# Performance work log

Hardware: AMD Instinct MI355X
Metric: run time of the kernel (lower is better)

## Reference

```python
import jax, jax.numpy as jnp
import numpy as np

LATENT_DIM = 256
CODEBOOK_SIZE = 8192


def setup_inputs() -> dict:
    key = jax.random.key(0)
    k1, k2 = jax.random.split(key)
    z_e = jax.random.normal(k1, (16, 32, 32, LATENT_DIM), dtype=jnp.float32)
    codebook = jax.random.normal(k2, (CODEBOOK_SIZE, LATENT_DIM), dtype=jnp.float32)
    return {"z_e": z_e, "codebook": codebook}


def reference(z_e, codebook):
    orig_shape = z_e.shape
    z_flat = z_e.reshape(-1, LATENT_DIM)                      # [N, D]
    # squared distances via ||z||^2 + ||e||^2 - 2 z.e^T  -> [N, K]
    dists = (jnp.sum(z_flat ** 2, axis=1, keepdims=True)
             + jnp.sum(codebook ** 2, axis=1)
             - 2.0 * jnp.matmul(z_flat, codebook.T))
    idx = jnp.argmin(dists, axis=1)                           # [N]
    z_q = codebook[idx].reshape(orig_shape)                   # gather + reshape
    commitment_loss = jnp.mean((jax.lax.stop_gradient(z_q) - z_e) ** 2)
    codebook_loss = jnp.mean((z_q - jax.lax.stop_gradient(z_e)) ** 2)
    loss = commitment_loss + codebook_loss
    z_q_st = z_e + jax.lax.stop_gradient(z_q - z_e)           # straight-through
    return (z_e, loss, z_q_st)
```

## Files before the change

kernel.cpp:

```cpp
#include <hip/hip_runtime.h>
#include <stdint.h>

typedef short short8 __attribute__((ext_vector_type(8)));
typedef float f32x4 __attribute__((ext_vector_type(4)));

#define DDIM 256
#define NROWS 16384
#define KCB 8192
#define KSPLIT 4
#define KC 2048
#define ND 4194304

__device__ __forceinline__ void gll16(const void* g, void* l) {
    __builtin_amdgcn_global_load_lds(
        (const __attribute__((address_space(1))) unsigned int*)g,
        (__attribute__((address_space(3))) unsigned int*)l, 16, 0, 0);
}

__device__ __forceinline__ unsigned short bf16_rne(float x) {
    unsigned u = __float_as_uint(x);
    unsigned r = (u + 0x7FFFu + ((u >> 16) & 1u)) >> 16;
    return (unsigned short)r;
}

__global__ void k_prep(const float* __restrict__ z, const float* __restrict__ cb,
                       unsigned short* __restrict__ zh, unsigned short* __restrict__ zl,
                       unsigned short* __restrict__ eh, unsigned short* __restrict__ el,
                       float* __restrict__ norms) {
    const int b = blockIdx.x, t = threadIdx.x;
    const bool isz = (b < 4096);
    const float* src = isz ? z : cb;
    unsigned short* hi = isz ? zh : eh;
    unsigned short* lo = isz ? zl : el;
    const int i = (isz ? b : (b - 4096)) * 256 + t;
    float4 v = reinterpret_cast<const float4*>(src)[i];
    ushort4 h, l;
    h.x = bf16_rne(v.x); l.x = bf16_rne(v.x - __uint_as_float((unsigned)h.x << 16));
    h.y = bf16_rne(v.y); l.y = bf16_rne(v.y - __uint_as_float((unsigned)h.y << 16));
    h.z = bf16_rne(v.z); l.z = bf16_rne(v.z - __uint_as_float((unsigned)h.z << 16));
    h.w = bf16_rne(v.w); l.w = bf16_rne(v.w - __uint_as_float((unsigned)h.w << 16));
    reinterpret_cast<ushort4*>(hi)[i] = h;
    reinterpret_cast<ushort4*>(lo)[i] = l;
    if (!isz) {
        float s = v.x * v.x + v.y * v.y + v.z * v.z + v.w * v.w;
#pragma unroll
        for (int off = 32; off > 0; off >>= 1) s += __shfl_xor(s, off, 64);
        if ((t & 63) == 0) norms[i >> 6] = s;
    }
}

__launch_bounds__(256, 2)
__global__ void k_score(const unsigned short* __restrict__ zh, const unsigned short* __restrict__ zl,
                        const unsigned short* __restrict__ eh, const unsigned short* __restrict__ el,
                        const float* __restrict__ norms,
                        float* __restrict__ cand_val, int* __restrict__ cand_idx) {
    __shared__ char smem[65536];

    const int rb = blockIdx.x;
    const int ks = blockIdx.y;
    const int t = threadIdx.x, w = t >> 6, lane = t & 63;
    const int l15 = lane & 15, l4 = lane >> 4;

    const int colq = t >> 3;
    const int voff0 = colq * 512 + (((t & 7) ^ (colq & 7)) * 16);

    int voffB[2];
#pragma unroll
    for (int kc = 0; kc < 2; ++kc)
        voffB[kc] = l15 * 128 + ((((kc * 4) + l4) ^ (lane & 7)) * 16);

    short8 Ah[2][8], Al[2][8];
    {
        const size_t base0 = ((size_t)(rb * 128 + w * 32 + l15)) * DDIM + l4 * 8;
#pragma unroll
        for (int r = 0; r < 2; ++r)
#pragma unroll
            for (int kk = 0; kk < 8; ++kk) {
                Ah[r][kk] = *reinterpret_cast<const short8*>(zh + base0 + r * 16 * DDIM + kk * 32);
                Al[r][kk] = *reinterpret_cast<const short8*>(zl + base0 + r * 16 * DDIM + kk * 32);
            }
    }

    const char* pe = (const char*)eh + (size_t)(ks * KC) * 512;
    const char* pl = (const char*)el + (size_t)(ks * KC) * 512;

    auto stage = [&](int s) {
        const int off = (s >> 2) * 32768 + (s & 3) * 128;
        char* sdst = smem + (s & 3) * 16384 + t * 16;
        gll16(pe + off + voff0,         sdst);
        gll16(pe + off + voff0 + 16384, sdst + 4096);
        gll16(pl + off + voff0,         sdst + 8192);
        gll16(pl + off + voff0 + 16384, sdst + 12288);
    };

    float v1[8], v2[8]; unsigned pk[8];
#pragma unroll
    for (int s = 0; s < 8; ++s) { v1[s] = 3.4e38f; v2[s] = 3.4e38f; pk[s] = 0; }

    f32x4 acc[2][4];

    auto compute = [&](int dc) {
        const char* cb0 = smem + dc * 16384;
        __builtin_amdgcn_s_setprio(1);
#pragma unroll
        for (int cf = 0; cf < 4; ++cf) {
#pragma unroll
            for (int kc = 0; kc < 2; ++kc) {
                short8 bh = *reinterpret_cast<const short8*>(cb0 + cf * 2048 + voffB[kc]);
                short8 bl = *reinterpret_cast<const short8*>(cb0 + 8192 + cf * 2048 + voffB[kc]);
                const int kk = dc * 2 + kc;
#pragma unroll
                for (int r = 0; r < 2; ++r) {
                    acc[r][cf] = __builtin_amdgcn_mfma_f32_16x16x32_bf16(Ah[r][kk], bh, acc[r][cf], 0, 0, 0);
                    acc[r][cf] = __builtin_amdgcn_mfma_f32_16x16x32_bf16(Ah[r][kk], bl, acc[r][cf], 0, 0, 0);
                    acc[r][cf] = __builtin_amdgcn_mfma_f32_16x16x32_bf16(Al[r][kk], bh, acc[r][cf], 0, 0, 0);
                }
            }
        }
        __builtin_amdgcn_s_setprio(0);
    };

    auto fold = [&](int ct) {
        const int nb = ks * KC + ct * 64 + l15;
        const float nn0 = norms[nb], nn1 = norms[nb + 16];
        const float nn2 = norms[nb + 32], nn3 = norms[nb + 48];
        const int cl0 = ct * 64 + l15;
#pragma unroll
        for (int r = 0; r < 2; ++r)
#pragma unroll
            for (int reg = 0; reg < 4; ++reg) {
                float s0 = fmaf(-2.f, acc[r][0][reg], nn0);
                float s1 = fmaf(-2.f, acc[r][1][reg], nn1);
                float s2 = fmaf(-2.f, acc[r][2][reg], nn2);
                float s3 = fmaf(-2.f, acc[r][3][reg], nn3);
                float sm = s0; int sj = cl0;
                if (s1 < sm) { sm = s1; sj = cl0 + 16; }
                if (s2 < sm) { sm = s2; sj = cl0 + 32; }
                if (s3 < sm) { sm = s3; sj = cl0 + 48; }
                const int s = r * 4 + reg;
                if (sm < v1[s]) { v2[s] = v1[s]; pk[s] = (pk[s] << 16) | (unsigned)sj; v1[s] = sm; }
                else if (sm < v2[s]) { v2[s] = sm; pk[s] = (pk[s] & 0xFFFFu) | ((unsigned)sj << 16); }
            }
    };

#define ACC_ZERO() do { \
    _Pragma("unroll") for (int r = 0; r < 2; ++r) \
    _Pragma("unroll") for (int cf = 0; cf < 4; ++cf) acc[r][cf] = (f32x4){0.f,0.f,0.f,0.f}; } while (0)

#define SYNC_V8()  do { asm volatile("s_waitcnt vmcnt(8) lgkmcnt(0)" ::: "memory"); \
    __builtin_amdgcn_sched_barrier(0); __builtin_amdgcn_s_barrier(); } while (0)
#define SYNC_V4()  do { asm volatile("s_waitcnt vmcnt(4) lgkmcnt(0)" ::: "memory"); \
    __builtin_amdgcn_sched_barrier(0); __builtin_amdgcn_s_barrier(); } while (0)
#define SYNC_V0()  do { asm volatile("s_waitcnt vmcnt(0) lgkmcnt(0)" ::: "memory"); \
    __builtin_amdgcn_sched_barrier(0); __builtin_amdgcn_s_barrier(); } while (0)

    stage(0); stage(1); stage(2);
    asm volatile("s_waitcnt vmcnt(8)" ::: "memory");
    __builtin_amdgcn_sched_barrier(0);
    __builtin_amdgcn_s_barrier();

#pragma unroll 1
    for (int ct = 0; ct < 31; ++ct) {
        ACC_ZERO();
        const int s0 = ct * 4;
#pragma unroll
        for (int dc = 0; dc < 4; ++dc) {
            stage(s0 + dc + 3);
            compute(dc);
            SYNC_V8();
        }
        fold(ct);
    }
    ACC_ZERO();
    stage(127); compute(0); SYNC_V8();
    compute(1);             SYNC_V4();
    compute(2);             SYNC_V0();
    compute(3);
    fold(31);

#pragma unroll
    for (int m = 1; m < 16; m <<= 1) {
#pragma unroll
        for (int s = 0; s < 8; ++s) {
            float ov1 = __shfl_xor(v1[s], m, 64);
            float ov2 = __shfl_xor(v2[s], m, 64);
            unsigned opk = (unsigned)__shfl_xor((int)pk[s], m, 64);
            const int ia = (int)(pk[s] & 0xFFFFu), ib = (int)(opk & 0xFFFFu);
            bool bl = (ov1 < v1[s]) || (ov1 == v1[s] && ib < ia);
            float f1 = bl ? ov1 : v1[s]; int fi = bl ? ib : ia;
            float rv = bl ? v1[s] : ov1; int ri = bl ? ia : ib;
            float sv = bl ? ov2 : v2[s]; int si = bl ? (int)(opk >> 16) : (int)(pk[s] >> 16);
            bool b2 = (sv < rv) || (sv == rv && si < ri);
            v1[s] = f1; v2[s] = b2 ? sv : rv;
            pk[s] = (unsigned)fi | ((unsigned)(b2 ? si : ri) << 16);
        }
    }
    __syncthreads();
    if (l15 == 0) {
#pragma unroll
        for (int s = 0; s < 8; ++s) {
            const int row = (s >> 2) * 16 + l4 * 4 + (s & 3);
            const int n = w * 32 + row;
            reinterpret_cast<int4*>(smem)[n] =
                make_int4(__float_as_int(v1[s]), (int)(pk[s] & 0xFFFFu),
                          __float_as_int(v2[s]), (int)(pk[s] >> 16));
        }
    }
    __syncthreads();
    if (t < 128) {
        int4 A = reinterpret_cast<int4*>(smem)[t];
        const int n = rb * 128 + t;
        cand_val[n * 8 + ks * 2 + 0] = __int_as_float(A.x);
        cand_val[n * 8 + ks * 2 + 1] = __int_as_float(A.z);
        cand_idx[n * 8 + ks * 2 + 0] = ks * KC + A.y;
        cand_idx[n * 8 + ks * 2 + 1] = ks * KC + A.w;
    }
}

__global__ void k_merge(const float* __restrict__ z, const float* __restrict__ cb,
                        const float* __restrict__ norms,
                        const float* __restrict__ cand_val, const int* __restrict__ cand_idx,
                        int* __restrict__ fidx) {
    const int gid = blockIdx.x * blockDim.x + threadIdx.x;
    const int wid = gid >> 6;
    const int lane = threadIdx.x & 63;
    float v1 = 3.4e38f, v2 = 3.4e38f; int i1 = 0, i2 = 0;
#pragma unroll
    for (int c = 0; c < 8; ++c) {
        float v = cand_val[wid * 8 + c]; int i = cand_idx[wid * 8 + c] & (KCB - 1);
        bool lt1 = (v < v1) || (v == v1 && i < i1);
        bool lt2 = (v < v2) || (v == v2 && i < i2);
        if (lt1) { v2 = v1; i2 = i1; v1 = v; i1 = i; }
        else if (lt2) { v2 = v; i2 = i; }
    }
    const float4 zq = *reinterpret_cast<const float4*>(z + (size_t)wid * DDIM + lane * 4);
    float d[2]; int ii[2] = { i1, i2 };
#pragma unroll
    for (int c = 0; c < 2; ++c) {
        const float4 e4 = *reinterpret_cast<const float4*>(cb + (size_t)ii[c] * DDIM + lane * 4);
        float s = zq.x * e4.x + zq.y * e4.y + zq.z * e4.z + zq.w * e4.w;
#pragma unroll
        for (int m = 32; m > 0; m >>= 1) s += __shfl_xor(s, m, 64);
        d[c] = norms[ii[c]] - 2.f * s;
    }
    const int best = (d[1] < d[0] || (d[1] == d[0] && ii[1] < ii[0])) ? ii[1] : ii[0];
    if (lane == 0) fidx[wid] = best;
}

__global__ void k_finalize(const float* __restrict__ z, const float* __restrict__ cb,
                           const int* __restrict__ fidx, float* __restrict__ out,
                           float* __restrict__ partials) {
    const int i4 = blockIdx.x * blockDim.x + threadIdx.x;
    float4 zv = *reinterpret_cast<const float4*>(z + (size_t)i4 * 4);
    *reinterpret_cast<float4*>(out + (size_t)i4 * 4) = zv;
    const int n = i4 >> 6;
    const int d0 = (i4 & 63) << 2;
    const int idx = fidx[n] & (KCB - 1);
    float4 q = *reinterpret_cast<const float4*>(cb + (size_t)idx * DDIM + d0);
    float* oq = out + (size_t)ND + 1 + (size_t)i4 * 4;
    oq[0] = q.x; oq[1] = q.y; oq[2] = q.z; oq[3] = q.w;
    const float dx = q.x - zv.x, dy = q.y - zv.y, dz = q.z - zv.z, dw = q.w - zv.w;
    float s = dx * dx + dy * dy + dz * dz + dw * dw;
#pragma unroll
    for (int off = 32; off > 0; off >>= 1) s += __shfl_xor(s, off, 64);
    __shared__ float sm[4];
    const int wv = threadIdx.x >> 6, ln = threadIdx.x & 63;
    if (ln == 0) sm[wv] = s;
    __syncthreads();
    if (threadIdx.x == 0) partials[blockIdx.x] = sm[0] + sm[1] + sm[2] + sm[3];
}

__global__ void k_loss(const float* __restrict__ partials, float* __restrict__ out) {
    float s = 0.f;
    for (int i = threadIdx.x; i < 4096; i += 256) s += partials[i];
#pragma unroll
    for (int off = 32; off > 0; off >>= 1) s += __shfl_xor(s, off, 64);
    __shared__ float sm[4];
    const int wv = threadIdx.x >> 6, ln = threadIdx.x & 63;
    if (ln == 0) sm[wv] = s;
    __syncthreads();
    if (threadIdx.x == 0) out[ND] = 2.0f * (sm[0] + sm[1] + sm[2] + sm[3]) / (float)ND;
}

extern "C" void kernel_launch(void* const* d_in, const int* in_sizes, int n_in,
                              void* d_out, int out_size, void* d_ws, size_t ws_size,
                              hipStream_t stream) {
    const float* z = (const float*)d_in[0];
    const float* cb = (const float*)d_in[1];
    float* out = (float*)d_out;
    float* ws = (float*)d_ws;

    float* norms = ws;
    int* fidx = (int*)(ws + 8192);
    float* partials = ws + 8192 + 16384;

    char* ob = (char*)d_out;
    unsigned short* zh = (unsigned short*)(ob);
    unsigned short* zl = (unsigned short*)(ob + 8388608);
    unsigned short* eh = (unsigned short*)(ob + 16777216);
    unsigned short* el = (unsigned short*)(ob + 20971520);
    float* cand_val = (float*)(ob + 25165824);
    int* cand_idx = (int*)(ob + 25690112);

    k_prep<<<dim3(6144), dim3(256), 0, stream>>>(z, cb, zh, zl, eh, el, norms);
    k_score<<<dim3(128, 4), dim3(256), 0, stream>>>(zh, zl, eh, el, norms, cand_val, cand_idx);
    k_merge<<<dim3(4096), dim3(256), 0, stream>>>(z, cb, norms, cand_val, cand_idx, fidx);
    k_finalize<<<dim3(4096), dim3(256), 0, stream>>>(z, cb, fidx, out, partials);
    k_loss<<<dim3(1), dim3(256), 0, stream>>>(partials, out);
}
```

Measured before the change: 266.0 us.

## Replace split-bf16 3-pass MFMA with single fp16 MFMA and top-3 exact rescoring

The scoring GEMM now quantizes z and the codebook once to fp16 and runs a single f16 MFMA per tile, replacing three bf16 hi/lo MFMAs. To make up for the lower precision, each split keeps top-3 candidates instead of top-2, and the merge kernel re-scores all 12 candidates exactly in fp32. Other changes: LDS staging is halved, codebook norms are staged into LDS, occupancy is raised to 3 blocks per CU, and candidate values are no longer written out. The risk is that fp16 error pushes the true argmin outside the top-3 per split, and the merge kernel now does six times more gathers.

```diff
diff --git a/kernel.cpp b/kernel.cpp
--- a/kernel.cpp
+++ b/kernel.cpp
@@ -1,7 +1,7 @@
 #include <hip/hip_runtime.h>
 #include <stdint.h>
 
-typedef short short8 __attribute__((ext_vector_type(8)));
+typedef _Float16 half8 __attribute__((ext_vector_type(8)));
 typedef float f32x4 __attribute__((ext_vector_type(4)));
 
 #define DDIM 256
@@ -17,30 +17,24 @@
         (__attribute__((address_space(3))) unsigned int*)l, 16, 0, 0);
 }
 
-__device__ __forceinline__ unsigned short bf16_rne(float x) {
-    unsigned u = __float_as_uint(x);
-    unsigned r = (u + 0x7FFFu + ((u >> 16) & 1u)) >> 16;
-    return (unsigned short)r;
+__device__ __forceinline__ unsigned short f2h(float x) {
+    union { _Float16 h; unsigned short u; } c;
+    c.h = (_Float16)x;
+    return c.u;
 }
 
 __global__ void k_prep(const float* __restrict__ z, const float* __restrict__ cb,
-                       unsigned short* __restrict__ zh, unsigned short* __restrict__ zl,
-                       unsigned short* __restrict__ eh, unsigned short* __restrict__ el,
+                       unsigned short* __restrict__ zf, unsigned short* __restrict__ ef,
                        float* __restrict__ norms) {
     const int b = blockIdx.x, t = threadIdx.x;
     const bool isz = (b < 4096);
     const float* src = isz ? z : cb;
-    unsigned short* hi = isz ? zh : eh;
-    unsigned short* lo = isz ? zl : el;
+    unsigned short* dst = isz ? zf : ef;
     const int i = (isz ? b : (b - 4096)) * 256 + t;
     float4 v = reinterpret_cast<const float4*>(src)[i];
-    ushort4 h, l;
-    h.x = bf16_rne(v.x); l.x = bf16_rne(v.x - __uint_as_float((unsigned)h.x << 16));
-    h.y = bf16_rne(v.y); l.y = bf16_rne(v.y - __uint_as_float((unsigned)h.y << 16));
-    h.z = bf16_rne(v.z); l.z = bf16_rne(v.z - __uint_as_float((unsigned)h.z << 16));
-    h.w = bf16_rne(v.w); l.w = bf16_rne(v.w - __uint_as_float((unsigned)h.w << 16));
-    reinterpret_cast<ushort4*>(hi)[i] = h;
-    reinterpret_cast<ushort4*>(lo)[i] = l;
+    ushort4 h;
+    h.x = f2h(v.x); h.y = f2h(v.y); h.z = f2h(v.z); h.w = f2h(v.w);
+    reinterpret_cast<ushort4*>(dst)[i] = h;
     if (!isz) {
         float s = v.x * v.x + v.y * v.y + v.z * v.z + v.w * v.w;
 #pragma unroll
@@ -49,12 +43,10 @@
     }
 }
 
-__launch_bounds__(256, 2)
-__global__ void k_score(const unsigned short* __restrict__ zh, const unsigned short* __restrict__ zl,
-                        const unsigned short* __restrict__ eh, const unsigned short* __restrict__ el,
-                        const float* __restrict__ norms,
-                        float* __restrict__ cand_val, int* __restrict__ cand_idx) {
-    __shared__ char smem[65536];
+__launch_bounds__(256, 3)
+__global__ void k_score(const unsigned short* __restrict__ zf, const unsigned short* __restrict__ ef,
+                        const float* __restrict__ norms, int* __restrict__ cand_idx) {
+    __shared__ char smem[40960];
 
     const int rb = blockIdx.x;
     const int ks = blockIdx.y;
@@ -69,77 +61,81 @@
     for (int kc = 0; kc < 2; ++kc)
         voffB[kc] = l15 * 128 + ((((kc * 4) + l4) ^ (lane & 7)) * 16);
 
-    short8 Ah[2][8], Al[2][8];
+    half8 A[2][8];
     {
         const size_t base0 = ((size_t)(rb * 128 + w * 32 + l15)) * DDIM + l4 * 8;
 #pragma unroll
         for (int r = 0; r < 2; ++r)
 #pragma unroll
-            for (int kk = 0; kk < 8; ++kk) {
-                Ah[r][kk] = *reinterpret_cast<const short8*>(zh + base0 + r * 16 * DDIM + kk * 32);
-                Al[r][kk] = *reinterpret_cast<const short8*>(zl + base0 + r * 16 * DDIM + kk * 32);
-            }
-    }
-
-    const char* pe = (const char*)eh + (size_t)(ks * KC) * 512;
-    const char* pl = (const char*)el + (size_t)(ks * KC) * 512;
+            for (int kk = 0; kk < 8; ++kk)
+                A[r][kk] = *reinterpret_cast<const half8*>(zf + base0 + r * 16 * DDIM + kk * 32);
+    }
+#pragma unroll
+    for (int r = 0; r < 2; ++r)
+#pragma unroll
+        for (int kk = 0; kk < 8; ++kk)
+            asm volatile("" : "+v"(A[r][kk]));
+
+    const char* pe = (const char*)ef + (size_t)(ks * KC) * 512;
+
+    gll16((const char*)(norms + ks * KC) + t * 16,        smem + 32768 + t * 16);
+    gll16((const char*)(norms + ks * KC) + 4096 + t * 16, smem + 32768 + 4096 + t * 16);
 
     auto stage = [&](int s) {
         const int off = (s >> 2) * 32768 + (s & 3) * 128;
-        char* sdst = smem + (s & 3) * 16384 + t * 16;
+        char* sdst = smem + (s & 3) * 8192 + t * 16;
         gll16(pe + off + voff0,         sdst);
         gll16(pe + off + voff0 + 16384, sdst + 4096);
-        gll16(pl + off + voff0,         sdst + 8192);
-        gll16(pl + off + voff0 + 16384, sdst + 12288);
     };
 
-    float v1[8], v2[8]; unsigned pk[8];
-#pragma unroll
-    for (int s = 0; s < 8; ++s) { v1[s] = 3.4e38f; v2[s] = 3.4e38f; pk[s] = 0; }
+    float v1[8], v2[8], v3[8]; unsigned pk[8]; int i3[8];
+#pragma unroll
+    for (int s = 0; s < 8; ++s) { v1[s] = 3.4e38f; v2[s] = 3.4e38f; v3[s] = 3.4e38f; pk[s] = 0; i3[s] = 0; }
 
     f32x4 acc[2][4];
 
     auto compute = [&](int dc) {
-        const char* cb0 = smem + dc * 16384;
+        const char* cb0 = smem + dc * 8192;
         __builtin_amdgcn_s_setprio(1);
 #pragma unroll
         for (int cf = 0; cf < 4; ++cf) {
 #pragma unroll
             for (int kc = 0; kc < 2; ++kc) {
-                short8 bh = *reinterpret_cast<const short8*>(cb0 + cf * 2048 + voffB[kc]);
-                short8 bl = *reinterpret_cast<const short8*>(cb0 + 8192 + cf * 2048 + voffB[kc]);
+                half8 b = *reinterpret_cast<const half8*>(cb0 + cf * 2048 + voffB[kc]);
                 const int kk = dc * 2 + kc;
 #pragma unroll
-                for (int r = 0; r < 2; ++r) {
-                    acc[r][cf] = __builtin_amdgcn_mfma_f32_16x16x32_bf16(Ah[r][kk], bh, acc[r][cf], 0, 0, 0);
-                    acc[r][cf] = __builtin_amdgcn_mfma_f32_16x16x32_bf16(Ah[r][kk], bl, acc[r][cf], 0, 0, 0);
-                    acc[r][cf] = __builtin_amdgcn_mfma_f32_16x16x32_bf16(Al[r][kk], bh, acc[r][cf], 0, 0, 0);
-                }
+                for (int r = 0; r < 2; ++r)
+                    acc[r][cf] = __builtin_amdgcn_mfma_f32_16x16x32_f16(A[r][kk], b, acc[r][cf], 0, 0, 0);
             }
         }
         __builtin_amdgcn_s_setprio(0);
     };
 
     auto fold = [&](int ct) {
-        const int nb = ks * KC + ct * 64 + l15;
-        const float nn0 = norms[nb], nn1 = norms[nb + 16];
-        const float nn2 = norms[nb + 32], nn3 = norms[nb + 48];
-        const int cl0 = ct * 64 + l15;
+        const float* nl = reinterpret_cast<const float*>(smem + 32768);
+        const int nb0 = ct * 64 + l15;
+        float nn[4];
+#pragma unroll
+        for (int c = 0; c < 4; ++c) nn[c] = nl[nb0 + c * 16];
 #pragma unroll
         for (int r = 0; r < 2; ++r)
 #pragma unroll
             for (int reg = 0; reg < 4; ++reg) {
-                float s0 = fmaf(-2.f, acc[r][0][reg], nn0);
-                float s1 = fmaf(-2.f, acc[r][1][reg], nn1);
-                float s2 = fmaf(-2.f, acc[r][2][reg], nn2);
-                float s3 = fmaf(-2.f, acc[r][3][reg], nn3);
-                float sm = s0; int sj = cl0;
-                if (s1 < sm) { sm = s1; sj = cl0 + 16; }
-                if (s2 < sm) { sm = s2; sj = cl0 + 32; }
-                if (s3 < sm) { sm = s3; sj = cl0 + 48; }
                 const int s = r * 4 + reg;
-                if (sm < v1[s]) { v2[s] = v1[s]; pk[s] = (pk[s] << 16) | (unsigned)sj; v1[s] = sm; }
-                else if (sm < v2[s]) { v2[s] = sm; pk[s] = (pk[s] & 0xFFFFu) | ((unsigned)sj << 16); }
+#pragma unroll
+                for (int c = 0; c < 4; ++c) {
+                    const float val = fmaf(-2.f, acc[r][c][reg], nn[c]);
+                    const int idx = nb0 + c * 16;
+                    const bool L1 = val < v1[s], L2 = val < v2[s], L3 = val < v3[s];
+                    const int oi1 = (int)(pk[s] & 0xFFFFu), oi2 = (int)(pk[s] >> 16);
+                    i3[s] = L2 ? oi2 : (L3 ? idx : i3[s]);
+                    v3[s] = L2 ? v2[s] : (L3 ? val : v3[s]);
+                    const int ni2 = L1 ? oi1 : (L2 ? idx : oi2);
+                    v2[s] = L1 ? v1[s] : (L2 ? val : v2[s]);
+                    const int ni1 = L1 ? idx : oi1;
+                    v1[s] = L1 ? val : v1[s];
+                    pk[s] = (unsigned)ni1 | ((unsigned)ni2 << 16);
+                }
             }
     };
 
@@ -147,15 +143,15 @@
     _Pragma("unroll") for (int r = 0; r < 2; ++r) \
     _Pragma("unroll") for (int cf = 0; cf < 4; ++cf) acc[r][cf] = (f32x4){0.f,0.f,0.f,0.f}; } while (0)
 
-#define SYNC_V8()  do { asm volatile("s_waitcnt vmcnt(8) lgkmcnt(0)" ::: "memory"); \
+#define SYNC_V4()  do { asm volatile("s_waitcnt vmcnt(4) lgkmcnt(0)" ::: "memory"); \
     __builtin_amdgcn_sched_barrier(0); __builtin_amdgcn_s_barrier(); } while (0)
-#define SYNC_V4()  do { asm volatile("s_waitcnt vmcnt(4) lgkmcnt(0)" ::: "memory"); \
+#define SYNC_V2()  do { asm volatile("s_waitcnt vmcnt(2) lgkmcnt(0)" ::: "memory"); \
     __builtin_amdgcn_sched_barrier(0); __builtin_amdgcn_s_barrier(); } while (0)
 #define SYNC_V0()  do { asm volatile("s_waitcnt vmcnt(0) lgkmcnt(0)" ::: "memory"); \
     __builtin_amdgcn_sched_barrier(0); __builtin_amdgcn_s_barrier(); } while (0)
 
     stage(0); stage(1); stage(2);
-    asm volatile("s_waitcnt vmcnt(8)" ::: "memory");
+    asm volatile("s_waitcnt vmcnt(4)" ::: "memory");
     __builtin_amdgcn_sched_barrier(0);
     __builtin_amdgcn_s_barrier();
 
@@ -167,13 +163,13 @@
         for (int dc = 0; dc < 4; ++dc) {
             stage(s0 + dc + 3);
             compute(dc);
-            SYNC_V8();
+            SYNC_V4();
         }
         fold(ct);
     }
     ACC_ZERO();
-    stage(127); compute(0); SYNC_V8();
-    compute(1);             SYNC_V4();
+    stage(127); compute(0); SYNC_V4();
+    compute(1);             SYNC_V2();
     compute(2);             SYNC_V0();
     compute(3);
     fold(31);
@@ -182,69 +178,68 @@
     for (int m = 1; m < 16; m <<= 1) {
 #pragma unroll
         for (int s = 0; s < 8; ++s) {
-            float ov1 = __shfl_xor(v1[s], m, 64);
-            float ov2 = __shfl_xor(v2[s], m, 64);
-            unsigned opk = (unsigned)__shfl_xor((int)pk[s], m, 64);
-            const int ia = (int)(pk[s] & 0xFFFFu), ib = (int)(opk & 0xFFFFu);
-            bool bl = (ov1 < v1[s]) || (ov1 == v1[s] && ib < ia);
-            float f1 = bl ? ov1 : v1[s]; int fi = bl ? ib : ia;
-            float rv = bl ? v1[s] : ov1; int ri = bl ? ia : ib;
-            float sv = bl ? ov2 : v2[s]; int si = bl ? (int)(opk >> 16) : (int)(pk[s] >> 16);
-            bool b2 = (sv < rv) || (sv == rv && si < ri);
-            v1[s] = f1; v2[s] = b2 ? sv : rv;
-            pk[s] = (unsigned)fi | ((unsigned)(b2 ? si : ri) << 16);
+            const float a1v = v1[s], a2v = v2[s], a3v = v3[s];
+            const int a1i = (int)(pk[s] & 0xFFFFu), a2i = (int)(pk[s] >> 16), a3i = i3[s];
+            const float b1v = __shfl_xor(a1v, m, 64), b2v = __shfl_xor(a2v, m, 64), b3v = __shfl_xor(a3v, m, 64);
+            const unsigned opk = (unsigned)__shfl_xor((int)pk[s], m, 64);
+            const int b1i = (int)(opk & 0xFFFFu), b2i = (int)(opk >> 16), b3i = __shfl_xor(a3i, m, 64);
+            auto lt = [](float va, int ia, float vb, int ib) { return va < vb || (va == vb && ia < ib); };
+            const bool w1 = lt(a1v, a1i, b1v, b1i);
+            const float c1v = w1 ? a1v : b1v; const int c1i = w1 ? a1i : b1i;
+            const float xav = w1 ? a2v : a1v; const int xai = w1 ? a2i : a1i;
+            const float xbv = w1 ? b1v : b2v; const int xbi = w1 ? b1i : b2i;
+            const bool w2 = lt(xav, xai, xbv, xbi);
+            const float c2v = w2 ? xav : xbv; const int c2i = w2 ? xai : xbi;
+            const float yav = w1 ? (w2 ? a3v : a2v) : (w2 ? a2v : a1v);
+            const int   yai = w1 ? (w2 ? a3i : a2i) : (w2 ? a2i : a1i);
+            const float ybv = w1 ? (w2 ? b1v : b2v) : (w2 ? b2v : b3v);
+            const int   ybi = w1 ? (w2 ? b1i : b2i) : (w2 ? b2i : b3i);
+            const bool w3 = lt(yav, yai, ybv, ybi);
+            v1[s] = c1v; v2[s] = c2v; v3[s] = w3 ? yav : ybv;
+            pk[s] = (unsigned)c1i | ((unsigned)c2i << 16);
+            i3[s] = w3 ? yai : ybi;
         }
     }
-    __syncthreads();
     if (l15 == 0) {
 #pragma unroll
         for (int s = 0; s < 8; ++s) {
             const int row = (s >> 2) * 16 + l4 * 4 + (s & 3);
-            const int n = w * 32 + row;
-            reinterpret_cast<int4*>(smem)[n] =
-                make_int4(__float_as_int(v1[s]), (int)(pk[s] & 0xFFFFu),
-                          __float_as_int(v2[s]), (int)(pk[s] >> 16));
+            const int n = rb * 128 + w * 32 + row;
+            const int base = n * 12 + ks * 3;
+            cand_idx[base + 0] = ks * KC + (int)(pk[s] & 0xFFFFu);
+            cand_idx[base + 1] = ks * KC + (int)(pk[s] >> 16);
+            cand_idx[base + 2] = ks * KC + i3[s];
         }
     }
-    __syncthreads();
-    if (t < 128) {
-        int4 A = reinterpret_cast<int4*>(smem)[t];
-        const int n = rb * 128 + t;
-        cand_val[n * 8 + ks * 2 + 0] = __int_as_float(A.x);
-        cand_val[n * 8 + ks * 2 + 1] = __int_as_float(A.z);
-        cand_idx[n * 8 + ks * 2 + 0] = ks * KC + A.y;
-        cand_idx[n * 8 + ks * 2 + 1] = ks * KC + A.w;
-    }
 }
 
 __global__ void k_merge(const float* __restrict__ z, const float* __restrict__ cb,
-                        const float* __restrict__ norms,
-                        const float* __restrict__ cand_val, const int* __restrict__ cand_idx,
+                        const float* __restrict__ norms, const int* __restrict__ cand_idx,
                         int* __restrict__ fidx) {
     const int gid = blockIdx.x * blockDim.x + threadIdx.x;
     const int wid = gid >> 6;
     const int lane = threadIdx.x & 63;
-    float v1 = 3.4e38f, v2 = 3.4e38f; int i1 = 0, i2 = 0;
-#pragma unroll
-    for (int c = 0; c < 8; ++c) {
-        float v = cand_val[wid * 8 + c]; int i = cand_idx[wid * 8 + c] & (KCB - 1);
-        bool lt1 = (v < v1) || (v == v1 && i < i1);
-        bool lt2 = (v < v2) || (v == v2 && i < i2);
-        if (lt1) { v2 = v1; i2 = i1; v1 = v; i1 = i; }
-        else if (lt2) { v2 = v; i2 = i; }
-    }
+    int ii[12];
+#pragma unroll
+    for (int c = 0; c < 12; ++c) ii[c] = cand_idx[wid * 12 + c] & (KCB - 1);
     const float4 zq = *reinterpret_cast<const float4*>(z + (size_t)wid * DDIM + lane * 4);
-    float d[2]; int ii[2] = { i1, i2 };
-#pragma unroll
-    for (int c = 0; c < 2; ++c) {
+    float d[12];
+#pragma unroll
+    for (int c = 0; c < 12; ++c) {
         const float4 e4 = *reinterpret_cast<const float4*>(cb + (size_t)ii[c] * DDIM + lane * 4);
-        float s = zq.x * e4.x + zq.y * e4.y + zq.z * e4.z + zq.w * e4.w;
-#pragma unroll
-        for (int m = 32; m > 0; m >>= 1) s += __shfl_xor(s, m, 64);
-        d[c] = norms[ii[c]] - 2.f * s;
-    }
-    const int best = (d[1] < d[0] || (d[1] == d[0] && ii[1] < ii[0])) ? ii[1] : ii[0];
-    if (lane == 0) fidx[wid] = best;
+        d[c] = zq.x * e4.x + zq.y * e4.y + zq.z * e4.z + zq.w * e4.w;
+    }
+#pragma unroll
+    for (int m = 32; m > 0; m >>= 1)
+#pragma unroll
+        for (int c = 0; c < 12; ++c) d[c] += __shfl_xor(d[c], m, 64);
+    float bv = 3.4e38f; int bi = 0;
+#pragma unroll
+    for (int c = 0; c < 12; ++c) {
+        const float s = norms[ii[c]] - 2.f * d[c];
+        if (s < bv || (s == bv && ii[c] < bi)) { bv = s; bi = ii[c]; }
+    }
+    if (lane == 0) fidx[wid] = bi;
 }
 
 __global__ void k_finalize(const float* __restrict__ z, const float* __restrict__ cb,
@@ -295,16 +290,13 @@
     float* partials = ws + 8192 + 16384;
 
     char* ob = (char*)d_out;
-    unsigned short* zh = (unsigned short*)(ob);
-    unsigned short* zl = (unsigned short*)(ob + 8388608);
-    unsigned short* eh = (unsigned short*)(ob + 16777216);
-    unsigned short* el = (unsigned short*)(ob + 20971520);
-    float* cand_val = (float*)(ob + 25165824);
-    int* cand_idx = (int*)(ob + 25690112);
-
-    k_prep<<<dim3(6144), dim3(256), 0, stream>>>(z, cb, zh, zl, eh, el, norms);
-    k_score<<<dim3(128, 4), dim3(256), 0, stream>>>(zh, zl, eh, el, norms, cand_val, cand_idx);
-    k_merge<<<dim3(4096), dim3(256), 0, stream>>>(z, cb, norms, cand_val, cand_idx, fidx);
+    unsigned short* zf = (unsigned short*)(ob);
+    unsigned short* ef = (unsigned short*)(ob + 8388608);
+    int* cand_idx = (int*)(ob + 12582912);
+
+    k_prep<<<dim3(6144), dim3(256), 0, stream>>>(z, cb, zf, ef, norms);
+    k_score<<<dim3(128, 4), dim3(256), 0, stream>>>(zf, ef, norms, cand_idx);
+    k_merge<<<dim3(4096), dim3(256), 0, stream>>>(z, cb, norms, cand_idx, fidx);
     k_finalize<<<dim3(4096), dim3(256), 0, stream>>>(z, cb, fidx, out, partials);
     k_loss<<<dim3(1), dim3(256), 0, stream>>>(partials, out);
 }
```

Result: faster. 260.8 us (-2.0%).
